# Performance work log

Measured on AMD Instinct MI355X. Metric: run time of the kernel, lower is better.

Reference implementation:

```python
import jax, jax.numpy as jnp
import numpy as np

CAP = 512  # per-expert capacity; mean tokens/expert = 4096*4/64 = 256, CAP = mean + ~16 sigma (no drops for seed 0)


def _moe_forward(hidden_states, gate_w, w13, w2, top_k):
    T, H = hidden_states.shape
    E = gate_w.shape[0]
    # --- gating: softmax over expert logits, then top-k (npu_moe_gating_top_k_softmax) ---
    logits = hidden_states @ gate_w.T                      # [T, E]
    probs = jax.nn.softmax(logits, axis=-1)
    topk_w, topk_idx = jax.lax.top_k(probs, top_k)         # [T, K]
    # norm_topk_prob=True and top_k > 1
    topk_w = topk_w / (topk_w.sum(axis=-1, keepdims=True) + 1e-20)
    # --- init_routing: compute each (token, slot)'s rank within its expert ---
    N = T * top_k
    flat_e = topk_idx.reshape(N)                           # [N] expert id per expanded row
    order = jnp.argsort(flat_e)                            # stable sort by expert
    sorted_e = flat_e[order]
    counts = jax.ops.segment_sum(jnp.ones((N,), jnp.int32), flat_e, num_segments=E)
    starts = jnp.cumsum(counts) - counts                   # [E] start offset of each expert group
    rank_sorted = jnp.arange(N, dtype=jnp.int32) - starts[sorted_e].astype(jnp.int32)
    rank = jnp.zeros((N,), jnp.int32).at[order].set(rank_sorted)  # within-expert position
    # --- dispatch into [E, CAP, H] buffers (token gather/scatter) ---
    x_rep = jnp.repeat(hidden_states, top_k, axis=0)       # [N, H]
    disp = jnp.zeros((E, CAP, H), hidden_states.dtype).at[flat_e, rank].set(x_rep)
    # --- grouped GEMM: SwiGLU expert FFN as batched matmuls ---
    h = jnp.einsum('ech,ehf->ecf', disp, w13)              # [E, CAP, 2I]
    g, u = jnp.split(h, 2, axis=-1)
    a = jax.nn.silu(g) * u                                 # [E, CAP, I]
    y = jnp.einsum('eci,eih->ech', a, w2)                  # [E, CAP, H]
    # --- finalize_routing: gather back and weighted combine ---
    out_rows = y[flat_e, rank]                             # [N, H]
    out = (out_rows.reshape(T, top_k, H) * topk_w[..., None]).sum(axis=1)
    return out


def setup_inputs() -> dict:
    key = jax.random.key(0)
    k1, k2, k3, k4 = jax.random.split(key, 4)
    T, H, E, I = 4096, 2048, 64, 768
    hidden_states = jax.random.normal(k1, (T, H), dtype=jnp.float32)
    gate_w = jax.random.normal(k2, (E, H), dtype=jnp.float32) * 0.02
    w13 = jax.random.normal(k3, (E, H, 2 * I), dtype=jnp.float32) * 0.02
    w2 = jax.random.normal(k4, (E, I, H), dtype=jnp.float32) * 0.02
    return {"hidden_states": hidden_states, "gate_w": gate_w, "w13": w13, "w2": w2, "top_k": 4}


def reference(hidden_states, gate_w, w13, w2, top_k):
    return _moe_forward(hidden_states, gate_w, w13, w2, top_k)
```

## Files before the change

### kernel.cpp

```cpp
#include <hip/hip_runtime.h>
#include <hip/hip_bf16.h>

#define T_TOK 4096
#define HDIM  2048
#define NEXP  64
#define IDIM  768
#define TOPK  4
#define CAPE  512
#define NFLAT (T_TOK*TOPK)

typedef __bf16        bf16x8 __attribute__((ext_vector_type(8)));
typedef float         f32x4  __attribute__((ext_vector_type(4)));
typedef unsigned int  u32x4  __attribute__((ext_vector_type(4)));

__device__ __forceinline__ unsigned short f2bf(float f) {
  __bf16 b = (__bf16)f;
  return __builtin_bit_cast(unsigned short, b);
}
__device__ __forceinline__ unsigned pack2(float lo, float hi) {
  return (unsigned)f2bf(lo) | ((unsigned)f2bf(hi) << 16);
}
__device__ __forceinline__ int swz(int row, int chunk) {
  return row*128 + (((chunk ^ (row & 7) ^ ((row >> 3) & 7)) & 7) << 4);
}
__device__ __forceinline__ void gload_lds16(const void* g, void* l) {
  __builtin_amdgcn_global_load_lds(
      (const __attribute__((address_space(1))) unsigned int*)g,
      (__attribute__((address_space(3))) unsigned int*)l, 16, 0, 0);
}

__global__ __launch_bounds__(256) void k_gating(
    const float* __restrict__ hs, const float* __restrict__ gw,
    unsigned short* __restrict__ hs_bf, int* __restrict__ tidx, float* __restrict__ tw)
{
  __shared__ float lg[16][64];
  const int tid = threadIdx.x;
  const int t0  = blockIdx.x * 16;

  {
    const f32x4* src = (const f32x4*)(hs + (size_t)t0 * HDIM);
    for (int i = tid; i < 16 * HDIM / 4; i += 256) {
      f32x4 v = src[i];
      ushort4 o;
      o.x = f2bf(v[0]); o.y = f2bf(v[1]); o.z = f2bf(v[2]); o.w = f2bf(v[3]);
      *(ushort4*)(hs_bf + (size_t)t0 * HDIM + (size_t)i * 4) = o;
    }
  }

  const int lane = tid & 63, wv = tid >> 6;
  {
    const f32x4* gr = (const f32x4*)(gw + (size_t)lane * HDIM);
    const f32x4* x0 = (const f32x4*)(hs + (size_t)(t0 + wv*4 + 0) * HDIM);
    const f32x4* x1 = (const f32x4*)(hs + (size_t)(t0 + wv*4 + 1) * HDIM);
    const f32x4* x2 = (const f32x4*)(hs + (size_t)(t0 + wv*4 + 2) * HDIM);
    const f32x4* x3 = (const f32x4*)(hs + (size_t)(t0 + wv*4 + 3) * HDIM);
    float a0=0.f, a1=0.f, a2=0.f, a3=0.f;
    for (int h = 0; h < HDIM/4; ++h) {
      f32x4 g = gr[h];
      f32x4 v0 = x0[h], v1 = x1[h], v2 = x2[h], v3 = x3[h];
      a0 += g[0]*v0[0] + g[1]*v0[1] + g[2]*v0[2] + g[3]*v0[3];
      a1 += g[0]*v1[0] + g[1]*v1[1] + g[2]*v1[2] + g[3]*v1[3];
      a2 += g[0]*v2[0] + g[1]*v2[1] + g[2]*v2[2] + g[3]*v2[3];
      a3 += g[0]*v3[0] + g[1]*v3[1] + g[2]*v3[2] + g[3]*v3[3];
    }
    lg[wv*4+0][lane] = a0;
    lg[wv*4+1][lane] = a1;
    lg[wv*4+2][lane] = a2;
    lg[wv*4+3][lane] = a3;
  }
  __syncthreads();

  if (tid < 16) {
    const int t = t0 + tid;
    unsigned long long chosen = 0ull;
    float bv[4]; int bi[4];
#pragma unroll
    for (int k = 0; k < 4; ++k) {
      float best = -1e30f; int b = 0;
      for (int e = 0; e < 64; ++e) {
        float v = lg[tid][e];
        if (!((chosen >> e) & 1ull) && v > best) { best = v; b = e; }
      }
      chosen |= 1ull << b; bv[k] = best; bi[k] = b;
    }
    float s = 0.f, w[4];
#pragma unroll
    for (int k = 0; k < 4; ++k) { w[k] = __expf(bv[k] - bv[0]); s += w[k]; }
    float inv = 1.f / s;
#pragma unroll
    for (int k = 0; k < 4; ++k) { tidx[t*4+k] = bi[k]; tw[t*4+k] = w[k] * inv; }
  }
}

__global__ __launch_bounds__(64) void k_count_rank(
    const int* __restrict__ tidx, int* __restrict__ rankb, int* __restrict__ counts)
{
  const int e = blockIdx.x;
  const int lane = threadIdx.x;
  int base = 0;
  for (int c = 0; c < NFLAT/64; ++c) {
    int n = c*64 + lane;
    bool m = (tidx[n] == e);
    unsigned long long mask = __ballot(m);
    if (m) rankb[n] = base + __popcll(mask & ((1ull << lane) - 1ull));
    base += __popcll(mask);
  }
  if (lane == 0) counts[e] = base;
}

__global__ __launch_bounds__(256) void k_build(
    const int* __restrict__ tidx, const int* __restrict__ rankb,
    const int* __restrict__ counts,
    int* __restrict__ starts, int* __restrict__ row_info, int* __restrict__ sortpos)
{
  __shared__ int s_starts[NEXP];
  if (threadIdx.x == 0) {
    int s = 0;
    for (int e = 0; e < NEXP; ++e) { s_starts[e] = s; starts[e] = s; s += counts[e]; }
  }
  __syncthreads();
  for (int n = threadIdx.x; n < NFLAT; n += 256) {
    int e = tidx[n], r = rankb[n];
    int sr = s_starts[e] + r;
    row_info[sr] = n;
    sortpos[n] = (r < CAPE) ? sr : -1;
  }
}

__global__ __launch_bounds__(256, 3) void k_gemm1(
    const unsigned short* __restrict__ hs_bf, const float* __restrict__ w13,
    const int* __restrict__ counts, const int* __restrict__ starts,
    const int* __restrict__ row_info, unsigned short* __restrict__ a_buf)
{
  const int nt = blockIdx.x;
  const int e  = blockIdx.y;
  const int count = min(counts[e], CAPE);
  if (count <= 0) return;
  const int nmt = (count + 127) >> 7;
  const int tid = threadIdx.x;
  const int estart = starts[e];

  __shared__ __align__(16) char lds[32768];

  const int lane = tid & 63, wv = tid >> 6;
  const int wr = wv >> 1, wc = wv & 1;

  const int bhalf = tid >> 7;
  const int t7 = tid & 127;
  const int bkg = t7 >> 4;
  const int bc4 = (t7 & 15) * 4;
  const float* w13e = w13 + (size_t)e * HDIM * (2*IDIM) + (size_t)bhalf*IDIM + (size_t)nt*64 + bc4;

  int srcch[4];
#pragma unroll
  for (int r = 0; r < 4; ++r)
    srcch[r] = (lane & 7) ^ (lane >> 3) ^ ((wv*4 + r) & 7);

  for (int mit = 0; mit < nmt; ++mit) {
    const int R0 = mit << 7;
    const int base_sorted = estart + R0;
    int tokp[4];
#pragma unroll
    for (int r = 0; r < 4; ++r) {
      int sr = base_sorted + wv*32 + r*8 + (lane >> 3);
      if (sr > NFLAT-1) sr = NFLAT-1;
      tokp[r] = row_info[sr] >> 2;
    }

    f32x4 accg[4][2], accu[4][2];
#pragma unroll
    for (int i = 0; i < 4; ++i)
#pragma unroll
      for (int j = 0; j < 2; ++j) { accg[i][j] = f32x4{0.f,0.f,0.f,0.f}; accu[i][j] = f32x4{0.f,0.f,0.f,0.f}; }

    for (int kt = 0; kt < HDIM/64; ++kt) {
#pragma unroll
      for (int r = 0; r < 4; ++r)
        gload_lds16(hs_bf + (size_t)tokp[r]*HDIM + kt*64 + srcch[r]*8,
                    lds + wv*4096 + r*1024 + lane*16);
      {
        const float* bp = w13e + (size_t)(kt*64 + bkg*8) * (2*IDIM);
        f32x4 f[8];
#pragma unroll
        for (int j = 0; j < 8; ++j) f[j] = *(const f32x4*)(bp + (size_t)j * (2*IDIM));
        char* Bh = lds + 16384 + bhalf*8192;
#pragma unroll
        for (int i = 0; i < 4; ++i) {
          u32x4 q;
          q[0] = pack2(f[0][i], f[1][i]);
          q[1] = pack2(f[2][i], f[3][i]);
          q[2] = pack2(f[4][i], f[5][i]);
          q[3] = pack2(f[6][i], f[7][i]);
          *(u32x4*)(Bh + swz(bc4 + i, bkg)) = q;
        }
      }
      __syncthreads();
      char* Bgl = lds + 16384;
      char* Bul = lds + 24576;
#pragma unroll
      for (int kfi = 0; kfi < 2; ++kfi) {
        const int ch = (kfi<<2) | (lane>>4);
        bf16x8 af[4], bg[2], bu[2];
#pragma unroll
        for (int m2 = 0; m2 < 4; ++m2)
          af[m2] = *(const bf16x8*)(lds + swz(wr*64 + m2*16 + (lane & 15), ch));
#pragma unroll
        for (int ni = 0; ni < 2; ++ni) {
          int col = wc*32 + ni*16 + (lane & 15);
          bg[ni] = *(const bf16x8*)(Bgl + swz(col, ch));
          bu[ni] = *(const bf16x8*)(Bul + swz(col, ch));
        }
#pragma unroll
        for (int m2 = 0; m2 < 4; ++m2)
#pragma unroll
          for (int ni = 0; ni < 2; ++ni) {
            accg[m2][ni] = __builtin_amdgcn_mfma_f32_16x16x32_bf16(af[m2], bg[ni], accg[m2][ni], 0, 0, 0);
            accu[m2][ni] = __builtin_amdgcn_mfma_f32_16x16x32_bf16(af[m2], bu[ni], accu[m2][ni], 0, 0, 0);
          }
      }
      __syncthreads();
    }

#pragma unroll
    for (int m2 = 0; m2 < 4; ++m2) {
#pragma unroll
      for (int j = 0; j < 4; ++j) {
        int rl = wr*64 + m2*16 + (lane >> 4)*4 + j;
        if (R0 + rl < count) {
          size_t rowoff = (size_t)(base_sorted + rl) * IDIM;
#pragma unroll
          for (int ni = 0; ni < 2; ++ni) {
            int col = nt*64 + wc*32 + ni*16 + (lane & 15);
            float g = accg[m2][ni][j], u = accu[m2][ni][j];
            float a = (g / (1.f + __expf(-g))) * u;
            a_buf[rowoff + col] = f2bf(a);
          }
        }
      }
    }
  }
}

__global__ __launch_bounds__(256, 3) void k_gemm2(
    const unsigned short* __restrict__ a_buf, const float* __restrict__ w2,
    const int* __restrict__ counts, const int* __restrict__ starts,
    unsigned short* __restrict__ y_buf)
{
  const int nt = blockIdx.x;
  const int e  = blockIdx.y;
  const int count = min(counts[e], CAPE);
  if (count <= 0) return;
  const int nmt = (count + 127) >> 7;
  const int tid = threadIdx.x;
  const int estart = starts[e];

  __shared__ __align__(16) char lds[32768];

  const int lane = tid & 63, wv = tid >> 6;
  const int wr = wv >> 1, wc = wv & 1;

  const int bkg = tid >> 5;
  const int bc4 = (tid & 31) * 4;
  const float* w2e = w2 + (size_t)e * IDIM * HDIM + (size_t)nt*128 + bc4;

  int srcch[4];
#pragma unroll
  for (int r = 0; r < 4; ++r)
    srcch[r] = (lane & 7) ^ (lane >> 3) ^ ((wv*4 + r) & 7);

  for (int mit = 0; mit < nmt; ++mit) {
    const int R0 = mit << 7;
    const int base_sorted = estart + R0;
    int srp[4];
#pragma unroll
    for (int r = 0; r < 4; ++r) {
      int sr = base_sorted + wv*32 + r*8 + (lane >> 3);
      srp[r] = (sr > NFLAT-1) ? (NFLAT-1) : sr;
    }

    f32x4 acc[4][4];
#pragma unroll
    for (int i = 0; i < 4; ++i)
#pragma unroll
      for (int j = 0; j < 4; ++j) acc[i][j] = f32x4{0.f,0.f,0.f,0.f};

    for (int kt = 0; kt < IDIM/64; ++kt) {
#pragma unroll
      for (int r = 0; r < 4; ++r)
        gload_lds16(a_buf + (size_t)srp[r]*IDIM + kt*64 + srcch[r]*8,
                    lds + wv*4096 + r*1024 + lane*16);
      {
        const float* bp = w2e + (size_t)(kt*64 + bkg*8) * HDIM;
        f32x4 f[8];
#pragma unroll
        for (int j = 0; j < 8; ++j) f[j] = *(const f32x4*)(bp + (size_t)j * HDIM);
        char* Bl = lds + 16384;
#pragma unroll
        for (int i = 0; i < 4; ++i) {
          u32x4 q;
          q[0] = pack2(f[0][i], f[1][i]);
          q[1] = pack2(f[2][i], f[3][i]);
          q[2] = pack2(f[4][i], f[5][i]);
          q[3] = pack2(f[6][i], f[7][i]);
          *(u32x4*)(Bl + swz(bc4 + i, bkg)) = q;
        }
      }
      __syncthreads();
      char* Bl = lds + 16384;
#pragma unroll
      for (int kfi = 0; kfi < 2; ++kfi) {
        const int ch = (kfi<<2) | (lane>>4);
        bf16x8 af[4], bb[4];
#pragma unroll
        for (int m2 = 0; m2 < 4; ++m2)
          af[m2] = *(const bf16x8*)(lds + swz(wr*64 + m2*16 + (lane & 15), ch));
#pragma unroll
        for (int ni = 0; ni < 4; ++ni)
          bb[ni] = *(const bf16x8*)(Bl + swz(wc*64 + ni*16 + (lane & 15), ch));
#pragma unroll
        for (int m2 = 0; m2 < 4; ++m2)
#pragma unroll
          for (int ni = 0; ni < 4; ++ni)
            acc[m2][ni] = __builtin_amdgcn_mfma_f32_16x16x32_bf16(af[m2], bb[ni], acc[m2][ni], 0, 0, 0);
      }
      __syncthreads();
    }

#pragma unroll
    for (int m2 = 0; m2 < 4; ++m2) {
#pragma unroll
      for (int j = 0; j < 4; ++j) {
        int rl = wr*64 + m2*16 + (lane >> 4)*4 + j;
        if (R0 + rl < count) {
          int sr = base_sorted + rl;
          unsigned short* yrow = y_buf + (size_t)sr * HDIM;
#pragma unroll
          for (int ni = 0; ni < 4; ++ni) {
            int col = nt*128 + wc*64 + ni*16 + (lane & 15);
            yrow[col] = f2bf(acc[m2][ni][j]);
          }
        }
      }
    }
  }
}

__global__ __launch_bounds__(256) void k_finalize(
    const unsigned short* __restrict__ y_buf, const int* __restrict__ sortpos,
    const float* __restrict__ tw, float* __restrict__ out)
{
  const int t = blockIdx.x;
  const int tid = threadIdx.x;
  float acc[8];
#pragma unroll
  for (int i = 0; i < 8; ++i) acc[i] = 0.f;
#pragma unroll
  for (int k = 0; k < 4; ++k) {
    int sp = sortpos[t*4+k];
    float w = tw[t*4+k];
    if (sp >= 0) {
      u32x4 v = *(const u32x4*)(y_buf + (size_t)sp * HDIM + tid*8);
#pragma unroll
      for (int q = 0; q < 4; ++q) {
        float lo = __builtin_bit_cast(float, v[q] << 16);
        float hi = __builtin_bit_cast(float, v[q] & 0xffff0000u);
        acc[2*q]   += w * lo;
        acc[2*q+1] += w * hi;
      }
    }
  }
  f32x4 o0 = {acc[0], acc[1], acc[2], acc[3]};
  f32x4 o1 = {acc[4], acc[5], acc[6], acc[7]};
  f32x4* o = (f32x4*)(out + (size_t)t * HDIM + tid*8);
  o[0] = o0;
  o[1] = o1;
}

extern "C" void kernel_launch(void* const* d_in, const int* in_sizes, int n_in,
                              void* d_out, int out_size, void* d_ws, size_t ws_size,
                              hipStream_t stream) {
  const float* hs  = (const float*)d_in[0];
  const float* gw  = (const float*)d_in[1];
  const float* w13 = (const float*)d_in[2];
  const float* w2  = (const float*)d_in[3];
  float* out = (float*)d_out;

  char* ws = (char*)d_ws;
  size_t off = 0;
  auto alloc = [&](size_t bytes) {
    off = (off + 255) & ~(size_t)255;
    char* p = ws + off;
    off += bytes;
    return p;
  };
  unsigned short* hs_bf = (unsigned short*)alloc((size_t)T_TOK * HDIM * 2);
  int*   tidx   = (int*)  alloc((size_t)NFLAT * 4);
  float* tw     = (float*)alloc((size_t)NFLAT * 4);
  int*   rankb  = (int*)  alloc((size_t)NFLAT * 4);
  int*   counts = (int*)  alloc((size_t)NEXP * 4);
  int*   starts = (int*)  alloc((size_t)NEXP * 4);
  int*   rinfo  = (int*)  alloc((size_t)NFLAT * 4);
  int*   sortp  = (int*)  alloc((size_t)NFLAT * 4);
  unsigned short* a_buf = (unsigned short*)alloc((size_t)NFLAT * IDIM * 2);
  unsigned short* y_buf = (unsigned short*)alloc((size_t)NFLAT * HDIM * 2);
  (void)ws_size; (void)in_sizes; (void)n_in; (void)out_size;

  k_gating<<<T_TOK/16, 256, 0, stream>>>(hs, gw, hs_bf, tidx, tw);
  k_count_rank<<<NEXP, 64, 0, stream>>>(tidx, rankb, counts);
  k_build<<<1, 256, 0, stream>>>(tidx, rankb, counts, starts, rinfo, sortp);
  k_gemm1<<<dim3(12, NEXP), 256, 0, stream>>>(hs_bf, w13, counts, starts, rinfo, a_buf);
  k_gemm2<<<dim3(16, NEXP), 256, 0, stream>>>(a_buf, w2, counts, starts, y_buf);
  k_finalize<<<T_TOK, 256, 0, stream>>>(y_buf, sortp, tw, out);
}
```

Before: 943.7 us.

## Enlarge grouped-GEMM M tile to 256 rows and remap blocks per XCD

Both expert GEMMs now use 256-row M tiles, with each wave owning 64 rows and the full N tile, instead of 128-row tiles on a 2x2 wave grid. The fp32 weight tile is therefore loaded and converted to bf16 once per 256 tokens instead of per 128, which halves the dominant weight traffic. The 2D grid is flattened and remapped so all N-tiles of one expert land on the same XCD, improving L2 sharing of the expert's activations. In exchange, LDS per block and accumulator registers double, which may lower occupancy under launch_bounds(256,3), and experts with few tokens waste more of each tile.

```diff
diff --git a/kernel.cpp b/kernel.cpp
--- a/kernel.cpp
+++ b/kernel.cpp
@@ -12,6 +12,7 @@
 typedef __bf16        bf16x8 __attribute__((ext_vector_type(8)));
 typedef float         f32x4  __attribute__((ext_vector_type(4)));
 typedef unsigned int  u32x4  __attribute__((ext_vector_type(4)));
+typedef unsigned int  u32x2  __attribute__((ext_vector_type(2)));
 
 __device__ __forceinline__ unsigned short f2bf(float f) {
   __bf16 b = (__bf16)f;
@@ -132,58 +133,59 @@
     const int* __restrict__ counts, const int* __restrict__ starts,
     const int* __restrict__ row_info, unsigned short* __restrict__ a_buf)
 {
-  const int nt = blockIdx.x;
-  const int e  = blockIdx.y;
+  const int b = blockIdx.x;
+  const int xcd = b & 7;
+  const int within = b >> 3;
+  const int e  = (within / 12) * 8 + xcd;
+  const int nt = within % 12;
   const int count = min(counts[e], CAPE);
   if (count <= 0) return;
-  const int nmt = (count + 127) >> 7;
+  const int nmt = (count + 255) >> 8;
   const int tid = threadIdx.x;
   const int estart = starts[e];
 
-  __shared__ __align__(16) char lds[32768];
+  __shared__ __align__(16) char lds[49152];
 
   const int lane = tid & 63, wv = tid >> 6;
-  const int wr = wv >> 1, wc = wv & 1;
-
-  const int bhalf = tid >> 7;
-  const int t7 = tid & 127;
-  const int bkg = t7 >> 4;
-  const int bc4 = (t7 & 15) * 4;
-  const float* w13e = w13 + (size_t)e * HDIM * (2*IDIM) + (size_t)bhalf*IDIM + (size_t)nt*64 + bc4;
-
-  int srcch[4];
-#pragma unroll
-  for (int r = 0; r < 4; ++r)
-    srcch[r] = (lane & 7) ^ (lane >> 3) ^ ((wv*4 + r) & 7);
+
+  const int bkg = tid >> 5;
+  const int n4  = (tid & 31) * 4;
+  const int gcol = (n4 < 64) ? (nt*64 + n4) : (IDIM + nt*64 + (n4 - 64));
+  const float* w13e = w13 + (size_t)e * HDIM * (2*IDIM) + gcol;
+
+  int srcch[8];
+#pragma unroll
+  for (int r = 0; r < 8; ++r)
+    srcch[r] = (lane & 7) ^ (lane >> 3) ^ ((wv*8 + r) & 7);
 
   for (int mit = 0; mit < nmt; ++mit) {
-    const int R0 = mit << 7;
+    const int R0 = mit << 8;
     const int base_sorted = estart + R0;
-    int tokp[4];
-#pragma unroll
-    for (int r = 0; r < 4; ++r) {
-      int sr = base_sorted + wv*32 + r*8 + (lane >> 3);
+    int tokp[8];
+#pragma unroll
+    for (int r = 0; r < 8; ++r) {
+      int sr = base_sorted + wv*64 + r*8 + (lane >> 3);
       if (sr > NFLAT-1) sr = NFLAT-1;
       tokp[r] = row_info[sr] >> 2;
     }
 
-    f32x4 accg[4][2], accu[4][2];
+    f32x4 accg[4][4], accu[4][4];
 #pragma unroll
     for (int i = 0; i < 4; ++i)
 #pragma unroll
-      for (int j = 0; j < 2; ++j) { accg[i][j] = f32x4{0.f,0.f,0.f,0.f}; accu[i][j] = f32x4{0.f,0.f,0.f,0.f}; }
+      for (int j = 0; j < 4; ++j) { accg[i][j] = f32x4{0.f,0.f,0.f,0.f}; accu[i][j] = f32x4{0.f,0.f,0.f,0.f}; }
 
     for (int kt = 0; kt < HDIM/64; ++kt) {
 #pragma unroll
-      for (int r = 0; r < 4; ++r)
+      for (int r = 0; r < 8; ++r)
         gload_lds16(hs_bf + (size_t)tokp[r]*HDIM + kt*64 + srcch[r]*8,
-                    lds + wv*4096 + r*1024 + lane*16);
+                    lds + wv*8192 + r*1024 + lane*16);
       {
         const float* bp = w13e + (size_t)(kt*64 + bkg*8) * (2*IDIM);
         f32x4 f[8];
 #pragma unroll
         for (int j = 0; j < 8; ++j) f[j] = *(const f32x4*)(bp + (size_t)j * (2*IDIM));
-        char* Bh = lds + 16384 + bhalf*8192;
+        char* Bl = lds + 32768;
 #pragma unroll
         for (int i = 0; i < 4; ++i) {
           u32x4 q;
@@ -191,29 +193,28 @@
           q[1] = pack2(f[2][i], f[3][i]);
           q[2] = pack2(f[4][i], f[5][i]);
           q[3] = pack2(f[6][i], f[7][i]);
-          *(u32x4*)(Bh + swz(bc4 + i, bkg)) = q;
+          *(u32x4*)(Bl + swz(n4 + i, bkg)) = q;
         }
       }
       __syncthreads();
-      char* Bgl = lds + 16384;
-      char* Bul = lds + 24576;
+      char* Bl = lds + 32768;
 #pragma unroll
       for (int kfi = 0; kfi < 2; ++kfi) {
         const int ch = (kfi<<2) | (lane>>4);
-        bf16x8 af[4], bg[2], bu[2];
+        bf16x8 af[4], bg[4], bu[4];
 #pragma unroll
         for (int m2 = 0; m2 < 4; ++m2)
-          af[m2] = *(const bf16x8*)(lds + swz(wr*64 + m2*16 + (lane & 15), ch));
-#pragma unroll
-        for (int ni = 0; ni < 2; ++ni) {
-          int col = wc*32 + ni*16 + (lane & 15);
-          bg[ni] = *(const bf16x8*)(Bgl + swz(col, ch));
-          bu[ni] = *(const bf16x8*)(Bul + swz(col, ch));
+          af[m2] = *(const bf16x8*)(lds + swz(wv*64 + m2*16 + (lane & 15), ch));
+#pragma unroll
+        for (int ni = 0; ni < 4; ++ni) {
+          int ic = ni*16 + (lane & 15);
+          bg[ni] = *(const bf16x8*)(Bl + swz(ic, ch));
+          bu[ni] = *(const bf16x8*)(Bl + swz(64 + ic, ch));
         }
 #pragma unroll
         for (int m2 = 0; m2 < 4; ++m2)
 #pragma unroll
-          for (int ni = 0; ni < 2; ++ni) {
+          for (int ni = 0; ni < 4; ++ni) {
             accg[m2][ni] = __builtin_amdgcn_mfma_f32_16x16x32_bf16(af[m2], bg[ni], accg[m2][ni], 0, 0, 0);
             accu[m2][ni] = __builtin_amdgcn_mfma_f32_16x16x32_bf16(af[m2], bu[ni], accu[m2][ni], 0, 0, 0);
           }
@@ -225,12 +226,12 @@
     for (int m2 = 0; m2 < 4; ++m2) {
 #pragma unroll
       for (int j = 0; j < 4; ++j) {
-        int rl = wr*64 + m2*16 + (lane >> 4)*4 + j;
+        int rl = wv*64 + m2*16 + (lane >> 4)*4 + j;
         if (R0 + rl < count) {
           size_t rowoff = (size_t)(base_sorted + rl) * IDIM;
 #pragma unroll
-          for (int ni = 0; ni < 2; ++ni) {
-            int col = nt*64 + wc*32 + ni*16 + (lane & 15);
+          for (int ni = 0; ni < 4; ++ni) {
+            int col = nt*64 + ni*16 + (lane & 15);
             float g = accg[m2][ni][j], u = accu[m2][ni][j];
             float a = (g / (1.f + __expf(-g))) * u;
             a_buf[rowoff + col] = f2bf(a);
@@ -246,55 +247,57 @@
     const int* __restrict__ counts, const int* __restrict__ starts,
     unsigned short* __restrict__ y_buf)
 {
-  const int nt = blockIdx.x;
-  const int e  = blockIdx.y;
+  const int b = blockIdx.x;
+  const int xcd = b & 7;
+  const int within = b >> 3;
+  const int e  = (within >> 4) * 8 + xcd;
+  const int nt = within & 15;
   const int count = min(counts[e], CAPE);
   if (count <= 0) return;
-  const int nmt = (count + 127) >> 7;
+  const int nmt = (count + 255) >> 8;
   const int tid = threadIdx.x;
   const int estart = starts[e];
 
-  __shared__ __align__(16) char lds[32768];
+  __shared__ __align__(16) char lds[49152];
 
   const int lane = tid & 63, wv = tid >> 6;
-  const int wr = wv >> 1, wc = wv & 1;
 
   const int bkg = tid >> 5;
-  const int bc4 = (tid & 31) * 4;
-  const float* w2e = w2 + (size_t)e * IDIM * HDIM + (size_t)nt*128 + bc4;
-
-  int srcch[4];
-#pragma unroll
-  for (int r = 0; r < 4; ++r)
-    srcch[r] = (lane & 7) ^ (lane >> 3) ^ ((wv*4 + r) & 7);
+  const int n4  = (tid & 31) * 4;
+  const float* w2e = w2 + (size_t)e * IDIM * HDIM + (size_t)nt*128 + n4;
+
+  int srcch[8];
+#pragma unroll
+  for (int r = 0; r < 8; ++r)
+    srcch[r] = (lane & 7) ^ (lane >> 3) ^ ((wv*8 + r) & 7);
 
   for (int mit = 0; mit < nmt; ++mit) {
-    const int R0 = mit << 7;
+    const int R0 = mit << 8;
     const int base_sorted = estart + R0;
-    int srp[4];
-#pragma unroll
-    for (int r = 0; r < 4; ++r) {
-      int sr = base_sorted + wv*32 + r*8 + (lane >> 3);
+    int srp[8];
+#pragma unroll
+    for (int r = 0; r < 8; ++r) {
+      int sr = base_sorted + wv*64 + r*8 + (lane >> 3);
       srp[r] = (sr > NFLAT-1) ? (NFLAT-1) : sr;
     }
 
-    f32x4 acc[4][4];
+    f32x4 acc[4][8];
 #pragma unroll
     for (int i = 0; i < 4; ++i)
 #pragma unroll
-      for (int j = 0; j < 4; ++j) acc[i][j] = f32x4{0.f,0.f,0.f,0.f};
+      for (int j = 0; j < 8; ++j) acc[i][j] = f32x4{0.f,0.f,0.f,0.f};
 
     for (int kt = 0; kt < IDIM/64; ++kt) {
 #pragma unroll
-      for (int r = 0; r < 4; ++r)
+      for (int r = 0; r < 8; ++r)
         gload_lds16(a_buf + (size_t)srp[r]*IDIM + kt*64 + srcch[r]*8,
-                    lds + wv*4096 + r*1024 + lane*16);
+                    lds + wv*8192 + r*1024 + lane*16);
       {
         const float* bp = w2e + (size_t)(kt*64 + bkg*8) * HDIM;
         f32x4 f[8];
 #pragma unroll
         for (int j = 0; j < 8; ++j) f[j] = *(const f32x4*)(bp + (size_t)j * HDIM);
-        char* Bl = lds + 16384;
+        char* Bl = lds + 32768;
 #pragma unroll
         for (int i = 0; i < 4; ++i) {
           u32x4 q;
@@ -302,25 +305,25 @@
           q[1] = pack2(f[2][i], f[3][i]);
           q[2] = pack2(f[4][i], f[5][i]);
           q[3] = pack2(f[6][i], f[7][i]);
-          *(u32x4*)(Bl + swz(bc4 + i, bkg)) = q;
+          *(u32x4*)(Bl + swz(n4 + i, bkg)) = q;
         }
       }
       __syncthreads();
-      char* Bl = lds + 16384;
+      char* Bl = lds + 32768;
 #pragma unroll
       for (int kfi = 0; kfi < 2; ++kfi) {
         const int ch = (kfi<<2) | (lane>>4);
-        bf16x8 af[4], bb[4];
+        bf16x8 af[4], bb[8];
 #pragma unroll
         for (int m2 = 0; m2 < 4; ++m2)
-          af[m2] = *(const bf16x8*)(lds + swz(wr*64 + m2*16 + (lane & 15), ch));
-#pragma unroll
-        for (int ni = 0; ni < 4; ++ni)
-          bb[ni] = *(const bf16x8*)(Bl + swz(wc*64 + ni*16 + (lane & 15), ch));
+          af[m2] = *(const bf16x8*)(lds + swz(wv*64 + m2*16 + (lane & 15), ch));
+#pragma unroll
+        for (int ni = 0; ni < 8; ++ni)
+          bb[ni] = *(const bf16x8*)(Bl + swz(ni*16 + (lane & 15), ch));
 #pragma unroll
         for (int m2 = 0; m2 < 4; ++m2)
 #pragma unroll
-          for (int ni = 0; ni < 4; ++ni)
+          for (int ni = 0; ni < 8; ++ni)
             acc[m2][ni] = __builtin_amdgcn_mfma_f32_16x16x32_bf16(af[m2], bb[ni], acc[m2][ni], 0, 0, 0);
       }
       __syncthreads();
@@ -330,13 +333,13 @@
     for (int m2 = 0; m2 < 4; ++m2) {
 #pragma unroll
       for (int j = 0; j < 4; ++j) {
-        int rl = wr*64 + m2*16 + (lane >> 4)*4 + j;
+        int rl = wv*64 + m2*16 + (lane >> 4)*4 + j;
         if (R0 + rl < count) {
           int sr = base_sorted + rl;
           unsigned short* yrow = y_buf + (size_t)sr * HDIM;
 #pragma unroll
-          for (int ni = 0; ni < 4; ++ni) {
-            int col = nt*128 + wc*64 + ni*16 + (lane & 15);
+          for (int ni = 0; ni < 8; ++ni) {
+            int col = nt*128 + ni*16 + (lane & 15);
             yrow[col] = f2bf(acc[m2][ni][j]);
           }
         }
@@ -408,7 +411,7 @@
   k_gating<<<T_TOK/16, 256, 0, stream>>>(hs, gw, hs_bf, tidx, tw);
   k_count_rank<<<NEXP, 64, 0, stream>>>(tidx, rankb, counts);
   k_build<<<1, 256, 0, stream>>>(tidx, rankb, counts, starts, rinfo, sortp);
-  k_gemm1<<<dim3(12, NEXP), 256, 0, stream>>>(hs_bf, w13, counts, starts, rinfo, a_buf);
-  k_gemm2<<<dim3(16, NEXP), 256, 0, stream>>>(a_buf, w2, counts, starts, y_buf);
+  k_gemm1<<<dim3(768), 256, 0, stream>>>(hs_bf, w13, counts, starts, rinfo, a_buf);
+  k_gemm2<<<dim3(1024), 256, 0, stream>>>(a_buf, w2, counts, starts, y_buf);
   k_finalize<<<T_TOK, 256, 0, stream>>>(y_buf, sortp, tw, out);
 }
```

Measured after the change: 1.499 ms. 1.59x slower.

## Pre-pack weights to swizzled bf16 tiles and double-buffer GEMM loads into LDS

Applied to the files above, without the earlier changes.

Adds conversion kernels that transform fp32 w13/w2 into bf16 tiles pre-swizzled in the LDS layout each call. The GEMMs then stream weight tiles with direct global-to-LDS loads into a double buffer, overlapping the next k-tile's loads with MFMA work, and use a flattened 1D grid. This removes per-m-tile fp32 loads and in-kernel conversion, at the cost of an extra full pass over the weights, extra workspace, and lower occupancy from doubled LDS.

```diff
diff --git a/kernel.cpp b/kernel.cpp
--- a/kernel.cpp
+++ b/kernel.cpp
@@ -20,8 +20,9 @@
 __device__ __forceinline__ unsigned pack2(float lo, float hi) {
   return (unsigned)f2bf(lo) | ((unsigned)f2bf(hi) << 16);
 }
+__device__ __forceinline__ int fswz(int row) { return ((row & 7) ^ ((row >> 3) & 7)) & 7; }
 __device__ __forceinline__ int swz(int row, int chunk) {
-  return row*128 + (((chunk ^ (row & 7) ^ ((row >> 3) & 7)) & 7) << 4);
+  return row*128 + (((chunk ^ fswz(row)) & 7) << 4);
 }
 __device__ __forceinline__ void gload_lds16(const void* g, void* l) {
   __builtin_amdgcn_global_load_lds(
@@ -127,29 +128,105 @@
   }
 }
 
-__global__ __launch_bounds__(256, 3) void k_gemm1(
-    const unsigned short* __restrict__ hs_bf, const float* __restrict__ w13,
+__device__ __forceinline__ int sAddr(int k, int c) {
+  return k*128 + (c ^ (((k >> 3) & 7) << 2));
+}
+__global__ __launch_bounds__(256) void k_conv13(
+    const float* __restrict__ w13, char* __restrict__ w13p)
+{
+  const int kt = blockIdx.x;
+  const int e  = blockIdx.y;
+  const int tid = threadIdx.x;
+  __shared__ float s[64*128];
+  const float* we = w13 + (size_t)e * HDIM * (2*IDIM) + (size_t)kt * 64 * (2*IDIM);
+
+  for (int cw = 0; cw < 12; ++cw) {
+    __syncthreads();
+#pragma unroll
+    for (int r = 0; r < 8; ++r) {
+      int idx = r*256 + tid;
+      int k = idx >> 5, c4 = (idx & 31) * 4;
+      f32x4 v = *(const f32x4*)(we + (size_t)k * (2*IDIM) + cw*128 + c4);
+      *(f32x4*)&s[sAddr(k, c4)] = v;
+    }
+    __syncthreads();
+    const int uhalf = (cw >= 6);
+    const int cwm = uhalf ? (cw - 6) : cw;
+#pragma unroll
+    for (int r = 0; r < 4; ++r) {
+      int o = r*256 + tid;
+      int t2 = o >> 9, oo = o & 511, nn = oo >> 3, s8 = oo & 7;
+      int n = nn + (uhalf ? 64 : 0);
+      int nt = cwm*2 + t2;
+      int ch = (s8 ^ fswz(n)) & 7;
+      int c = t2*64 + nn;
+      int k0 = ch*8;
+      u32x4 q;
+      q[0] = pack2(s[sAddr(k0+0, c)], s[sAddr(k0+1, c)]);
+      q[1] = pack2(s[sAddr(k0+2, c)], s[sAddr(k0+3, c)]);
+      q[2] = pack2(s[sAddr(k0+4, c)], s[sAddr(k0+5, c)]);
+      q[3] = pack2(s[sAddr(k0+6, c)], s[sAddr(k0+7, c)]);
+      *(u32x4*)(w13p + ((((size_t)e*32 + kt)*12 + nt) << 14) + n*128 + s8*16) = q;
+    }
+  }
+}
+
+__global__ __launch_bounds__(256) void k_conv2(
+    const float* __restrict__ w2, char* __restrict__ w2p)
+{
+  const int kt = blockIdx.x;
+  const int e  = blockIdx.y;
+  const int tid = threadIdx.x;
+  __shared__ float s[64*128];
+  const float* we = w2 + (size_t)e * IDIM * HDIM + (size_t)kt * 64 * HDIM;
+
+  for (int nt = 0; nt < 16; ++nt) {
+    __syncthreads();
+#pragma unroll
+    for (int r = 0; r < 8; ++r) {
+      int idx = r*256 + tid;
+      int k = idx >> 5, c4 = (idx & 31) * 4;
+      f32x4 v = *(const f32x4*)(we + (size_t)k * HDIM + nt*128 + c4);
+      *(f32x4*)&s[sAddr(k, c4)] = v;
+    }
+    __syncthreads();
+#pragma unroll
+    for (int r = 0; r < 4; ++r) {
+      int o = r*256 + tid;
+      int n = o >> 3, s8 = o & 7;
+      int ch = (s8 ^ fswz(n)) & 7;
+      int k0 = ch*8;
+      u32x4 q;
+      q[0] = pack2(s[sAddr(k0+0, n)], s[sAddr(k0+1, n)]);
+      q[1] = pack2(s[sAddr(k0+2, n)], s[sAddr(k0+3, n)]);
+      q[2] = pack2(s[sAddr(k0+4, n)], s[sAddr(k0+5, n)]);
+      q[3] = pack2(s[sAddr(k0+6, n)], s[sAddr(k0+7, n)]);
+      *(u32x4*)(w2p + ((((size_t)e*12 + kt)*16 + nt) << 14) + n*128 + s8*16) = q;
+    }
+  }
+}
+
+__global__ __launch_bounds__(256, 2) void k_gemm1(
+    const unsigned short* __restrict__ hs_bf, const char* __restrict__ w13p,
     const int* __restrict__ counts, const int* __restrict__ starts,
     const int* __restrict__ row_info, unsigned short* __restrict__ a_buf)
 {
-  const int nt = blockIdx.x;
-  const int e  = blockIdx.y;
+  const int b = blockIdx.x;
+  const int e  = b / 12;
+  const int nt = b % 12;
   const int count = min(counts[e], CAPE);
   if (count <= 0) return;
   const int nmt = (count + 127) >> 7;
   const int tid = threadIdx.x;
   const int estart = starts[e];
-
-  __shared__ __align__(16) char lds[32768];
+  const int NK = HDIM/64;
+
+  __shared__ __align__(16) char lds[2*32768];
 
   const int lane = tid & 63, wv = tid >> 6;
   const int wr = wv >> 1, wc = wv & 1;
 
-  const int bhalf = tid >> 7;
-  const int t7 = tid & 127;
-  const int bkg = t7 >> 4;
-  const int bc4 = (t7 & 15) * 4;
-  const float* w13e = w13 + (size_t)e * HDIM * (2*IDIM) + (size_t)bhalf*IDIM + (size_t)nt*64 + bc4;
+  const char* wtile = w13p + (((size_t)e*32)*12 + nt) * 16384;
 
   int srcch[4];
 #pragma unroll
@@ -173,42 +250,39 @@
 #pragma unroll
       for (int j = 0; j < 2; ++j) { accg[i][j] = f32x4{0.f,0.f,0.f,0.f}; accu[i][j] = f32x4{0.f,0.f,0.f,0.f}; }
 
-    for (int kt = 0; kt < HDIM/64; ++kt) {
+    auto STAGE = [&](int buf, int kt) {
+      char* Al = lds + buf*32768;
+      char* Bl = Al + 16384;
 #pragma unroll
       for (int r = 0; r < 4; ++r)
         gload_lds16(hs_bf + (size_t)tokp[r]*HDIM + kt*64 + srcch[r]*8,
-                    lds + wv*4096 + r*1024 + lane*16);
-      {
-        const float* bp = w13e + (size_t)(kt*64 + bkg*8) * (2*IDIM);
-        f32x4 f[8];
-#pragma unroll
-        for (int j = 0; j < 8; ++j) f[j] = *(const f32x4*)(bp + (size_t)j * (2*IDIM));
-        char* Bh = lds + 16384 + bhalf*8192;
-#pragma unroll
-        for (int i = 0; i < 4; ++i) {
-          u32x4 q;
-          q[0] = pack2(f[0][i], f[1][i]);
-          q[1] = pack2(f[2][i], f[3][i]);
-          q[2] = pack2(f[4][i], f[5][i]);
-          q[3] = pack2(f[6][i], f[7][i]);
-          *(u32x4*)(Bh + swz(bc4 + i, bkg)) = q;
-        }
-      }
+                    Al + wv*4096 + r*1024 + lane*16);
+      const char* bt = wtile + (size_t)kt * (12*16384);
+#pragma unroll
+      for (int r = 0; r < 4; ++r)
+        gload_lds16(bt + (r*256 + tid)*16, Bl + (r*256 + tid)*16);
+    };
+
+    __syncthreads();
+    STAGE(0, 0);
+    int cur = 0;
+    for (int kt = 0; kt < NK; ++kt) {
       __syncthreads();
-      char* Bgl = lds + 16384;
-      char* Bul = lds + 24576;
+      if (kt+1 < NK) STAGE(cur^1, kt+1);
+      char* Al = lds + cur*32768;
+      char* Bl = Al + 16384;
 #pragma unroll
       for (int kfi = 0; kfi < 2; ++kfi) {
         const int ch = (kfi<<2) | (lane>>4);
         bf16x8 af[4], bg[2], bu[2];
 #pragma unroll
         for (int m2 = 0; m2 < 4; ++m2)
-          af[m2] = *(const bf16x8*)(lds + swz(wr*64 + m2*16 + (lane & 15), ch));
+          af[m2] = *(const bf16x8*)(Al + swz(wr*64 + m2*16 + (lane & 15), ch));
 #pragma unroll
         for (int ni = 0; ni < 2; ++ni) {
-          int col = wc*32 + ni*16 + (lane & 15);
-          bg[ni] = *(const bf16x8*)(Bgl + swz(col, ch));
-          bu[ni] = *(const bf16x8*)(Bul + swz(col, ch));
+          int ic = wc*32 + ni*16 + (lane & 15);
+          bg[ni] = *(const bf16x8*)(Bl + swz(ic, ch));
+          bu[ni] = *(const bf16x8*)(Bl + swz(64 + ic, ch));
         }
 #pragma unroll
         for (int m2 = 0; m2 < 4; ++m2)
@@ -218,7 +292,7 @@
             accu[m2][ni] = __builtin_amdgcn_mfma_f32_16x16x32_bf16(af[m2], bu[ni], accu[m2][ni], 0, 0, 0);
           }
       }
-      __syncthreads();
+      cur ^= 1;
     }
 
 #pragma unroll
@@ -241,27 +315,27 @@
   }
 }
 
-__global__ __launch_bounds__(256, 3) void k_gemm2(
-    const unsigned short* __restrict__ a_buf, const float* __restrict__ w2,
+__global__ __launch_bounds__(256, 2) void k_gemm2(
+    const unsigned short* __restrict__ a_buf, const char* __restrict__ w2p,
     const int* __restrict__ counts, const int* __restrict__ starts,
     unsigned short* __restrict__ y_buf)
 {
-  const int nt = blockIdx.x;
-  const int e  = blockIdx.y;
+  const int b = blockIdx.x;
+  const int e  = b >> 4;
+  const int nt = b & 15;
   const int count = min(counts[e], CAPE);
   if (count <= 0) return;
   const int nmt = (count + 127) >> 7;
   const int tid = threadIdx.x;
   const int estart = starts[e];
-
-  __shared__ __align__(16) char lds[32768];
+  const int NK = IDIM/64;
+
+  __shared__ __align__(16) char lds[2*32768];
 
   const int lane = tid & 63, wv = tid >> 6;
   const int wr = wv >> 1, wc = wv & 1;
 
-  const int bkg = tid >> 5;
-  const int bc4 = (tid & 31) * 4;
-  const float* w2e = w2 + (size_t)e * IDIM * HDIM + (size_t)nt*128 + bc4;
+  const char* wtile = w2p + (((size_t)e*12)*16 + nt) * 16384;
 
   int srcch[4];
 #pragma unroll
@@ -284,36 +358,34 @@
 #pragma unroll
       for (int j = 0; j < 4; ++j) acc[i][j] = f32x4{0.f,0.f,0.f,0.f};
 
-    for (int kt = 0; kt < IDIM/64; ++kt) {
+    auto STAGE = [&](int buf, int kt) {
+      char* Al = lds + buf*32768;
+      char* Bl = Al + 16384;
 #pragma unroll
       for (int r = 0; r < 4; ++r)
         gload_lds16(a_buf + (size_t)srp[r]*IDIM + kt*64 + srcch[r]*8,
-                    lds + wv*4096 + r*1024 + lane*16);
-      {
-        const float* bp = w2e + (size_t)(kt*64 + bkg*8) * HDIM;
-        f32x4 f[8];
-#pragma unroll
-        for (int j = 0; j < 8; ++j) f[j] = *(const f32x4*)(bp + (size_t)j * HDIM);
-        char* Bl = lds + 16384;
-#pragma unroll
-        for (int i = 0; i < 4; ++i) {
-          u32x4 q;
-          q[0] = pack2(f[0][i], f[1][i]);
-          q[1] = pack2(f[2][i], f[3][i]);
-          q[2] = pack2(f[4][i], f[5][i]);
-          q[3] = pack2(f[6][i], f[7][i]);
-          *(u32x4*)(Bl + swz(bc4 + i, bkg)) = q;
-        }
-      }
+                    Al + wv*4096 + r*1024 + lane*16);
+      const char* bt = wtile + (size_t)kt * (16*16384);
+#pragma unroll
+      for (int r = 0; r < 4; ++r)
+        gload_lds16(bt + (r*256 + tid)*16, Bl + (r*256 + tid)*16);
+    };
+
+    __syncthreads();
+    STAGE(0, 0);
+    int cur = 0;
+    for (int kt = 0; kt < NK; ++kt) {
       __syncthreads();
-      char* Bl = lds + 16384;
+      if (kt+1 < NK) STAGE(cur^1, kt+1);
+      char* Al = lds + cur*32768;
+      char* Bl = Al + 16384;
 #pragma unroll
       for (int kfi = 0; kfi < 2; ++kfi) {
         const int ch = (kfi<<2) | (lane>>4);
         bf16x8 af[4], bb[4];
 #pragma unroll
         for (int m2 = 0; m2 < 4; ++m2)
-          af[m2] = *(const bf16x8*)(lds + swz(wr*64 + m2*16 + (lane & 15), ch));
+          af[m2] = *(const bf16x8*)(Al + swz(wr*64 + m2*16 + (lane & 15), ch));
 #pragma unroll
         for (int ni = 0; ni < 4; ++ni)
           bb[ni] = *(const bf16x8*)(Bl + swz(wc*64 + ni*16 + (lane & 15), ch));
@@ -323,7 +395,7 @@
           for (int ni = 0; ni < 4; ++ni)
             acc[m2][ni] = __builtin_amdgcn_mfma_f32_16x16x32_bf16(af[m2], bb[ni], acc[m2][ni], 0, 0, 0);
       }
-      __syncthreads();
+      cur ^= 1;
     }
 
 #pragma unroll
@@ -403,12 +475,16 @@
   int*   sortp  = (int*)  alloc((size_t)NFLAT * 4);
   unsigned short* a_buf = (unsigned short*)alloc((size_t)NFLAT * IDIM * 2);
   unsigned short* y_buf = (unsigned short*)alloc((size_t)NFLAT * HDIM * 2);
+  char* w13p = (char*)alloc((size_t)NEXP * 32 * 12 * 16384);
+  char* w2p  = (char*)alloc((size_t)NEXP * 12 * 16 * 16384);
   (void)ws_size; (void)in_sizes; (void)n_in; (void)out_size;
 
+  k_conv13<<<dim3(32, NEXP), 256, 0, stream>>>(w13, w13p);
+  k_conv2 <<<dim3(12, NEXP), 256, 0, stream>>>(w2, w2p);
   k_gating<<<T_TOK/16, 256, 0, stream>>>(hs, gw, hs_bf, tidx, tw);
   k_count_rank<<<NEXP, 64, 0, stream>>>(tidx, rankb, counts);
   k_build<<<1, 256, 0, stream>>>(tidx, rankb, counts, starts, rinfo, sortp);
-  k_gemm1<<<dim3(12, NEXP), 256, 0, stream>>>(hs_bf, w13, counts, starts, rinfo, a_buf);
-  k_gemm2<<<dim3(16, NEXP), 256, 0, stream>>>(a_buf, w2, counts, starts, y_buf);
+  k_gemm1<<<dim3(12*NEXP), 256, 0, stream>>>(hs_bf, w13p, counts, starts, rinfo, a_buf);
+  k_gemm2<<<dim3(16*NEXP), 256, 0, stream>>>(a_buf, w2p, counts, starts, y_buf);
   k_finalize<<<T_TOK, 256, 0, stream>>>(y_buf, sortp, tw, out);
 }
```

Result: slower. 970.8 us (+2.9%).

## Double-buffer grouped GEMMs with async global-to-LDS loads and 256-row tiles

Applied to the files above, without the earlier changes.

Both expert GEMM kernels now use 512-thread blocks covering 256 rows. Activation and raw fp32 weight tiles are double-buffered in LDS through global_load_lds, so the next K-tile's loads overlap the current tile's MFMA work. The fp32-to-bf16 weight conversion now reads from the LDS staging buffer instead of going through registers from global memory. This uses about 144KB of LDS per block, which limits occupancy to one block per CU, and it adds manual waitcnt and barrier synchronization.

```diff
diff --git a/kernel.cpp b/kernel.cpp
--- a/kernel.cpp
+++ b/kernel.cpp
@@ -20,8 +20,9 @@
 __device__ __forceinline__ unsigned pack2(float lo, float hi) {
   return (unsigned)f2bf(lo) | ((unsigned)f2bf(hi) << 16);
 }
+__device__ __forceinline__ int fswz(int row) { return ((row & 7) ^ ((row >> 3) & 7)) & 7; }
 __device__ __forceinline__ int swz(int row, int chunk) {
-  return row*128 + (((chunk ^ (row & 7) ^ ((row >> 3) & 7)) & 7) << 4);
+  return row*128 + (((chunk ^ fswz(row)) & 7) << 4);
 }
 __device__ __forceinline__ void gload_lds16(const void* g, void* l) {
   __builtin_amdgcn_global_load_lds(
@@ -127,37 +128,40 @@
   }
 }
 
-__global__ __launch_bounds__(256, 3) void k_gemm1(
+__global__ __launch_bounds__(512, 1) void k_gemm1(
     const unsigned short* __restrict__ hs_bf, const float* __restrict__ w13,
     const int* __restrict__ counts, const int* __restrict__ starts,
     const int* __restrict__ row_info, unsigned short* __restrict__ a_buf)
 {
-  const int nt = blockIdx.x;
-  const int e  = blockIdx.y;
+  const int b = blockIdx.x;
+  const int e  = b / 12;
+  const int nt = b % 12;
   const int count = min(counts[e], CAPE);
   if (count <= 0) return;
-  const int nmt = (count + 127) >> 7;
+  const int nmt = (count + 255) >> 8;
   const int tid = threadIdx.x;
   const int estart = starts[e];
-
-  __shared__ __align__(16) char lds[32768];
+  const int NK = HDIM/64;
+
+  __shared__ __align__(16) char lds[147456];
 
   const int lane = tid & 63, wv = tid >> 6;
   const int wr = wv >> 1, wc = wv & 1;
 
-  const int bhalf = tid >> 7;
-  const int t7 = tid & 127;
-  const int bkg = t7 >> 4;
-  const int bc4 = (t7 & 15) * 4;
-  const float* w13e = w13 + (size_t)e * HDIM * (2*IDIM) + (size_t)bhalf*IDIM + (size_t)nt*64 + bc4;
-
   int srcch[4];
 #pragma unroll
   for (int r = 0; r < 4; ++r)
     srcch[r] = (lane & 7) ^ (lane >> 3) ^ ((wv*4 + r) & 7);
 
+  const int n4 = (lane & 31) * 4;
+  const int gcol = (n4 < 64) ? (nt*64 + n4) : (IDIM + nt*64 + (n4 - 64));
+  const float* w13e = w13 + (size_t)e * HDIM * (2*IDIM) + gcol;
+
+  const int pn = tid >> 2;
+  const int ps = (tid & 3) * 2;
+
   for (int mit = 0; mit < nmt; ++mit) {
-    const int R0 = mit << 7;
+    const int R0 = mit << 8;
     const int base_sorted = estart + R0;
     int tokp[4];
 #pragma unroll
@@ -173,52 +177,76 @@
 #pragma unroll
       for (int j = 0; j < 2; ++j) { accg[i][j] = f32x4{0.f,0.f,0.f,0.f}; accu[i][j] = f32x4{0.f,0.f,0.f,0.f}; }
 
-    for (int kt = 0; kt < HDIM/64; ++kt) {
+    auto STAGE = [&](int p, int kt) {
+      char* Al = lds + p*32768;
+      char* Rl = lds + 65536 + p*32768;
 #pragma unroll
       for (int r = 0; r < 4; ++r)
         gload_lds16(hs_bf + (size_t)tokp[r]*HDIM + kt*64 + srcch[r]*8,
-                    lds + wv*4096 + r*1024 + lane*16);
+                    Al + wv*4096 + r*1024 + lane*16);
+#pragma unroll
+      for (int r = 0; r < 4; ++r)
+        gload_lds16(w13e + (size_t)(kt*64 + wv*8 + r*2 + (lane>>5)) * (2*IDIM),
+                    Rl + (wv*8 + r*2 + (lane>>5))*512 + (lane & 31)*16);
+    };
+
+    STAGE(0, 0);
+    for (int kt = 0; kt < NK; ++kt) {
+      const int p = kt & 1;
+      if (kt+1 < NK) {
+        STAGE(p^1, kt+1);
+        asm volatile("s_waitcnt vmcnt(8)" ::: "memory");
+      } else {
+        asm volatile("s_waitcnt vmcnt(0)" ::: "memory");
+      }
+      __builtin_amdgcn_s_barrier();
+
       {
-        const float* bp = w13e + (size_t)(kt*64 + bkg*8) * (2*IDIM);
-        f32x4 f[8];
-#pragma unroll
-        for (int j = 0; j < 8; ++j) f[j] = *(const f32x4*)(bp + (size_t)j * (2*IDIM));
-        char* Bh = lds + 16384 + bhalf*8192;
-#pragma unroll
-        for (int i = 0; i < 4; ++i) {
-          u32x4 q;
-          q[0] = pack2(f[0][i], f[1][i]);
-          q[1] = pack2(f[2][i], f[3][i]);
-          q[2] = pack2(f[4][i], f[5][i]);
-          q[3] = pack2(f[6][i], f[7][i]);
-          *(u32x4*)(Bh + swz(bc4 + i, bkg)) = q;
-        }
-      }
-      __syncthreads();
-      char* Bgl = lds + 16384;
-      char* Bul = lds + 24576;
+        const char* Rl = lds + 65536 + p*32768;
+        char* Bpk = lds + 131072;
+        float pf[16];
+#pragma unroll
+        for (int j = 0; j < 16; ++j)
+          pf[j] = *(const float*)(Rl + (ps*8 + j)*512 + pn*4);
+        u32x4 q0, q1;
+        q0[0] = pack2(pf[0],pf[1]);  q0[1] = pack2(pf[2],pf[3]);
+        q0[2] = pack2(pf[4],pf[5]);  q0[3] = pack2(pf[6],pf[7]);
+        q1[0] = pack2(pf[8],pf[9]);  q1[1] = pack2(pf[10],pf[11]);
+        q1[2] = pack2(pf[12],pf[13]); q1[3] = pack2(pf[14],pf[15]);
+        *(u32x4*)(Bpk + swz(pn, ps))   = q0;
+        *(u32x4*)(Bpk + swz(pn, ps+1)) = q1;
+      }
+      bf16x8 af[2][4];
+      {
+        const char* Al = lds + p*32768;
+#pragma unroll
+        for (int kfi = 0; kfi < 2; ++kfi)
+#pragma unroll
+          for (int m2 = 0; m2 < 4; ++m2)
+            af[kfi][m2] = *(const bf16x8*)(Al + swz(wr*64 + m2*16 + (lane & 15), (kfi<<2)|(lane>>4)));
+      }
+      asm volatile("s_waitcnt lgkmcnt(0)" ::: "memory");
+      __builtin_amdgcn_s_barrier();
+
+      const char* Bpk = lds + 131072;
 #pragma unroll
       for (int kfi = 0; kfi < 2; ++kfi) {
         const int ch = (kfi<<2) | (lane>>4);
-        bf16x8 af[4], bg[2], bu[2];
+        bf16x8 bg[2], bu[2];
+#pragma unroll
+        for (int ni = 0; ni < 2; ++ni) {
+          int ic = wc*32 + ni*16 + (lane & 15);
+          bg[ni] = *(const bf16x8*)(Bpk + swz(ic, ch));
+          bu[ni] = *(const bf16x8*)(Bpk + swz(64 + ic, ch));
+        }
 #pragma unroll
         for (int m2 = 0; m2 < 4; ++m2)
-          af[m2] = *(const bf16x8*)(lds + swz(wr*64 + m2*16 + (lane & 15), ch));
-#pragma unroll
-        for (int ni = 0; ni < 2; ++ni) {
-          int col = wc*32 + ni*16 + (lane & 15);
-          bg[ni] = *(const bf16x8*)(Bgl + swz(col, ch));
-          bu[ni] = *(const bf16x8*)(Bul + swz(col, ch));
-        }
-#pragma unroll
-        for (int m2 = 0; m2 < 4; ++m2)
 #pragma unroll
           for (int ni = 0; ni < 2; ++ni) {
-            accg[m2][ni] = __builtin_amdgcn_mfma_f32_16x16x32_bf16(af[m2], bg[ni], accg[m2][ni], 0, 0, 0);
-            accu[m2][ni] = __builtin_amdgcn_mfma_f32_16x16x32_bf16(af[m2], bu[ni], accu[m2][ni], 0, 0, 0);
+            accg[m2][ni] = __builtin_amdgcn_mfma_f32_16x16x32_bf16(af[kfi][m2], bg[ni], accg[m2][ni], 0, 0, 0);
+            accu[m2][ni] = __builtin_amdgcn_mfma_f32_16x16x32_bf16(af[kfi][m2], bu[ni], accu[m2][ni], 0, 0, 0);
           }
       }
-      __syncthreads();
     }
 
 #pragma unroll
@@ -241,35 +269,39 @@
   }
 }
 
-__global__ __launch_bounds__(256, 3) void k_gemm2(
+__global__ __launch_bounds__(512, 1) void k_gemm2(
     const unsigned short* __restrict__ a_buf, const float* __restrict__ w2,
     const int* __restrict__ counts, const int* __restrict__ starts,
     unsigned short* __restrict__ y_buf)
 {
-  const int nt = blockIdx.x;
-  const int e  = blockIdx.y;
+  const int b = blockIdx.x;
+  const int e  = b >> 4;
+  const int nt = b & 15;
   const int count = min(counts[e], CAPE);
   if (count <= 0) return;
-  const int nmt = (count + 127) >> 7;
+  const int nmt = (count + 255) >> 8;
   const int tid = threadIdx.x;
   const int estart = starts[e];
-
-  __shared__ __align__(16) char lds[32768];
+  const int NK = IDIM/64;
+
+  __shared__ __align__(16) char lds[147456];
 
   const int lane = tid & 63, wv = tid >> 6;
   const int wr = wv >> 1, wc = wv & 1;
 
-  const int bkg = tid >> 5;
-  const int bc4 = (tid & 31) * 4;
-  const float* w2e = w2 + (size_t)e * IDIM * HDIM + (size_t)nt*128 + bc4;
-
   int srcch[4];
 #pragma unroll
   for (int r = 0; r < 4; ++r)
     srcch[r] = (lane & 7) ^ (lane >> 3) ^ ((wv*4 + r) & 7);
 
+  const int n4 = (lane & 31) * 4;
+  const float* w2e = w2 + (size_t)e * IDIM * HDIM + (size_t)nt*128 + n4;
+
+  const int pn = tid >> 2;
+  const int ps = (tid & 3) * 2;
+
   for (int mit = 0; mit < nmt; ++mit) {
-    const int R0 = mit << 7;
+    const int R0 = mit << 8;
     const int base_sorted = estart + R0;
     int srp[4];
 #pragma unroll
@@ -284,46 +316,71 @@
 #pragma unroll
       for (int j = 0; j < 4; ++j) acc[i][j] = f32x4{0.f,0.f,0.f,0.f};
 
-    for (int kt = 0; kt < IDIM/64; ++kt) {
+    auto STAGE = [&](int p, int kt) {
+      char* Al = lds + p*32768;
+      char* Rl = lds + 65536 + p*32768;
 #pragma unroll
       for (int r = 0; r < 4; ++r)
         gload_lds16(a_buf + (size_t)srp[r]*IDIM + kt*64 + srcch[r]*8,
-                    lds + wv*4096 + r*1024 + lane*16);
+                    Al + wv*4096 + r*1024 + lane*16);
+#pragma unroll
+      for (int r = 0; r < 4; ++r)
+        gload_lds16(w2e + (size_t)(kt*64 + wv*8 + r*2 + (lane>>5)) * HDIM,
+                    Rl + (wv*8 + r*2 + (lane>>5))*512 + (lane & 31)*16);
+    };
+
+    STAGE(0, 0);
+    for (int kt = 0; kt < NK; ++kt) {
+      const int p = kt & 1;
+      if (kt+1 < NK) {
+        STAGE(p^1, kt+1);
+        asm volatile("s_waitcnt vmcnt(8)" ::: "memory");
+      } else {
+        asm volatile("s_waitcnt vmcnt(0)" ::: "memory");
+      }
+      __builtin_amdgcn_s_barrier();
+
       {
-        const float* bp = w2e + (size_t)(kt*64 + bkg*8) * HDIM;
-        f32x4 f[8];
-#pragma unroll
-        for (int j = 0; j < 8; ++j) f[j] = *(const f32x4*)(bp + (size_t)j * HDIM);
-        char* Bl = lds + 16384;
-#pragma unroll
-        for (int i = 0; i < 4; ++i) {
-          u32x4 q;
-          q[0] = pack2(f[0][i], f[1][i]);
-          q[1] = pack2(f[2][i], f[3][i]);
-          q[2] = pack2(f[4][i], f[5][i]);
-          q[3] = pack2(f[6][i], f[7][i]);
-          *(u32x4*)(Bl + swz(bc4 + i, bkg)) = q;
-        }
-      }
-      __syncthreads();
-      char* Bl = lds + 16384;
+        const char* Rl = lds + 65536 + p*32768;
+        char* Bpk = lds + 131072;
+        float pf[16];
+#pragma unroll
+        for (int j = 0; j < 16; ++j)
+          pf[j] = *(const float*)(Rl + (ps*8 + j)*512 + pn*4);
+        u32x4 q0, q1;
+        q0[0] = pack2(pf[0],pf[1]);  q0[1] = pack2(pf[2],pf[3]);
+        q0[2] = pack2(pf[4],pf[5]);  q0[3] = pack2(pf[6],pf[7]);
+        q1[0] = pack2(pf[8],pf[9]);  q1[1] = pack2(pf[10],pf[11]);
+        q1[2] = pack2(pf[12],pf[13]); q1[3] = pack2(pf[14],pf[15]);
+        *(u32x4*)(Bpk + swz(pn, ps))   = q0;
+        *(u32x4*)(Bpk + swz(pn, ps+1)) = q1;
+      }
+      bf16x8 af[2][4];
+      {
+        const char* Al = lds + p*32768;
+#pragma unroll
+        for (int kfi = 0; kfi < 2; ++kfi)
+#pragma unroll
+          for (int m2 = 0; m2 < 4; ++m2)
+            af[kfi][m2] = *(const bf16x8*)(Al + swz(wr*64 + m2*16 + (lane & 15), (kfi<<2)|(lane>>4)));
+      }
+      asm volatile("s_waitcnt lgkmcnt(0)" ::: "memory");
+      __builtin_amdgcn_s_barrier();
+
+      const char* Bpk = lds + 131072;
 #pragma unroll
       for (int kfi = 0; kfi < 2; ++kfi) {
         const int ch = (kfi<<2) | (lane>>4);
-        bf16x8 af[4], bb[4];
+        bf16x8 bb[4];
+#pragma unroll
+        for (int ni = 0; ni < 4; ++ni)
+          bb[ni] = *(const bf16x8*)(Bpk + swz(wc*64 + ni*16 + (lane & 15), ch));
 #pragma unroll
         for (int m2 = 0; m2 < 4; ++m2)
-          af[m2] = *(const bf16x8*)(lds + swz(wr*64 + m2*16 + (lane & 15), ch));
-#pragma unroll
-        for (int ni = 0; ni < 4; ++ni)
-          bb[ni] = *(const bf16x8*)(Bl + swz(wc*64 + ni*16 + (lane & 15), ch));
-#pragma unroll
-        for (int m2 = 0; m2 < 4; ++m2)
 #pragma unroll
           for (int ni = 0; ni < 4; ++ni)
-            acc[m2][ni] = __builtin_amdgcn_mfma_f32_16x16x32_bf16(af[m2], bb[ni], acc[m2][ni], 0, 0, 0);
-      }
-      __syncthreads();
+            acc[m2][ni] = __builtin_amdgcn_mfma_f32_16x16x32_bf16(af[kfi][m2], bb[ni], acc[m2][ni], 0, 0, 0);
+      }
     }
 
 #pragma unroll
@@ -408,7 +465,7 @@
   k_gating<<<T_TOK/16, 256, 0, stream>>>(hs, gw, hs_bf, tidx, tw);
   k_count_rank<<<NEXP, 64, 0, stream>>>(tidx, rankb, counts);
   k_build<<<1, 256, 0, stream>>>(tidx, rankb, counts, starts, rinfo, sortp);
-  k_gemm1<<<dim3(12, NEXP), 256, 0, stream>>>(hs_bf, w13, counts, starts, rinfo, a_buf);
-  k_gemm2<<<dim3(16, NEXP), 256, 0, stream>>>(a_buf, w2, counts, starts, y_buf);
+  k_gemm1<<<dim3(12*NEXP), 512, 0, stream>>>(hs_bf, w13, counts, starts, rinfo, a_buf);
+  k_gemm2<<<dim3(16*NEXP), 512, 0, stream>>>(a_buf, w2, counts, starts, y_buf);
   k_finalize<<<T_TOK, 256, 0, stream>>>(y_buf, sortp, tw, out);
 }
```

Measured after the change: 843.2 us. 1.12x faster.
